# Performance work log

Measured on AMD Instinct MI355X. Metric: run time of the kernel, lower is better.

## Reference

```python
import jax, jax.numpy as jnp
import numpy as np
import math

B, H, L, DK = 4, 16, 4096, 64
LK0 = 4096
LOG_LK = int(math.log(LK0))  # 8
LOG_L = int(math.log(L))     # 8
NC = 3
D_MODEL = H * DK             # 1024


def setup_inputs() -> dict:
    key = jax.random.key(0)
    ks = jax.random.split(key, 20)
    s = 0.02  # small init scale for stability of softmax/clustering
    f = jnp.float32
    return dict(
        Q=jax.random.normal(ks[0], (B, H, L, DK), f),
        K=jax.random.normal(ks[1], (B, H, LK0, DK), f),
        V=jax.random.normal(ks[2], (B, H, LK0, DK), f),
        shrink_k_w=jax.random.normal(ks[3], (LOG_LK, LK0), f) * s,
        shrink_k_b=jax.random.normal(ks[4], (LOG_LK,), f) * s,
        shrink_v_w=jax.random.normal(ks[5], (LOG_LK, LK0), f) * s,
        shrink_v_b=jax.random.normal(ks[6], (LOG_LK,), f) * s,
        shrink_q_w=jax.random.normal(ks[7], (LOG_L, L), f) * s,
        shrink_q_b=jax.random.normal(ks[8], (LOG_L,), f) * s,
        pk_w=jax.random.normal(ks[9], (NC, LOG_LK * D_MODEL), f) * s,
        pk_b=jax.random.normal(ks[10], (NC,), f) * s,
        pq_w=jax.random.normal(ks[11], (NC, LOG_L * D_MODEL), f) * s,
        pq_b=jax.random.normal(ks[12], (NC,), f) * s,
        qp_w=jax.random.normal(ks[13], (NC, NC), f) * s,
        qp_b=jax.random.normal(ks[14], (NC,), f) * s,
        kp_w=jax.random.normal(ks[15], (NC, NC), f) * s,
        kp_b=jax.random.normal(ks[16], (NC,), f) * s,
    )


def reference(Q, K, V, shrink_k_w, shrink_k_b, shrink_v_w, shrink_v_b,
              shrink_q_w, shrink_q_b, pk_w, pk_b, pq_w, pq_b,
              qp_w, qp_b, kp_w, kp_b):
    b, h, l, d_k = Q.shape
    # shrink along sequence axis (Linear over seq after permute in torch)
    Ks = jnp.einsum('bhkd,mk->bhmd', K, shrink_k_w) + shrink_k_b[None, None, :, None]
    Vs = jnp.einsum('bhkd,mk->bhmd', V, shrink_v_w) + shrink_v_b[None, None, :, None]
    Qs = jnp.einsum('bhqd,mq->bhmd', Q, shrink_q_w) + shrink_q_b[None, None, :, None]
    lk = Ks.shape[2]  # = LOG_LK
    # cluster logits -> soft assignments
    ckp = jax.nn.relu(Ks.reshape(b, -1) @ pk_w.T + pk_b)
    cqp = jax.nn.relu(Qs.reshape(b, -1) @ pq_w.T + pq_b)
    cluster_q = jax.nn.softmax(cqp @ qp_w.T + qp_b, axis=-1)
    cluster_k = jax.nn.softmax(ckp @ kp_w.T + kp_b, axis=-1)
    mu = jnp.mean(cluster_q, axis=0)
    sigma = jax.nn.softplus(jnp.std(cluster_k, axis=0, ddof=1))  # torch.std is unbiased
    logp = -0.5 * jnp.square((cluster_k - mu) / sigma) - jnp.log(sigma) - 0.5 * jnp.log(2.0 * jnp.pi)
    # CrossEntropyLoss with soft targets: -mean_b sum_c target*log_softmax(input)
    ce = jnp.mean(-jnp.sum(cluster_q * jax.nn.log_softmax(cluster_q, axis=-1), axis=-1))
    loss = -jnp.mean(logp) + ce

    inds_q = jnp.argmax(cluster_q, axis=-1)  # [b]
    inds_k = jnp.argmax(cluster_k, axis=-1)  # [b]
    # get_group masks whole batches whose cluster == i+1 (per-batch constant mask;
    # the reshape round-trip in the original is an identity on [b,h,seq,d])
    mask_tril = jnp.tril(jnp.ones((l, lk), dtype=bool))  # True positions get -1e9
    nc = qp_b.shape[0]
    scores_center = jnp.zeros((nc, b, h, l, lk), Q.dtype)
    row_idx = jnp.broadcast_to(inds_q[:, None, None], (b, h, l))  # q_ind[:,:,:,0]
    bi = jnp.arange(b)[:, None, None]
    hi = jnp.arange(h)[None, :, None]
    scale = 1.0 / jnp.sqrt(jnp.asarray(d_k, Q.dtype))
    for i in range(nc):
        gQ = jnp.where((inds_q != i + 1)[:, None, None, None], Q, 0.0)
        gK = jnp.where((inds_k != i + 1)[:, None, None, None], Ks, 0.0)
        s = jnp.einsum('bhqd,bhkd->bhqk', gQ, gK) * scale  # [b,h,l,lk]
        s = jnp.where(mask_tril, -1e9, s)
        # original repeats gK lk times along a c-axis, softmaxes, then means over c:
        # all c-copies are identical, so mean over c == the per-copy value; then [0]
        sm0 = jax.nn.softmax(s, axis=-1)[0]  # [h,l,lk] (batch 0, as in original)
        scores_center = scores_center.at[i, bi, hi, row_idx, :].set(
            jnp.broadcast_to(sm0, (b, h, l, lk)))
    final_score = jnp.max(scores_center, axis=0)  # [b,h,l,lk]
    attn = jax.nn.softmax(final_score, axis=-1)
    context = jnp.einsum('bhqk,bhkd->bhqd', attn, Vs)
    return context, loss
```

## Files before the change

### kernel.cpp

```cpp
#include <hip/hip_runtime.h>
#include <hip/hip_bf16.h>
#include <math.h>

#define BB   4
#define HH   16
#define LL   4096
#define DKK  64
#define MM   8
#define NCC  3
#define BH   (BB*HH)
#define NCHUNK 8
#define ROWS_PER_CHUNK (LL/NCHUNK)
#define NSLOT 4
#define CTX_ELEMS (BB*HH*LL*DKK)

#define DOTS_OFF (3*BH*NSLOT*512)

__global__ __launch_bounds__(256, 6) void shrink_kernel(
    const float* __restrict__ Q, const float* __restrict__ K,
    const float* __restrict__ V,
    const float* __restrict__ skw, const float* __restrict__ svw,
    const float* __restrict__ sqw,
    float* __restrict__ ws)
{
    __shared__ float wlds[MM * ROWS_PER_CHUNK];
    float* red = wlds;

    int bx    = blockIdx.x;
    int input = bx >> 9;
    int rem   = bx & 511;
    int bh    = rem >> 3;
    int chunk = rem & 7;

    const float* X; const float* W;
    if (input == 0)      { X = K; W = skw; }
    else if (input == 1) { X = V; W = svw; }
    else                 { X = Q; W = sqw; }

    int t  = threadIdx.x;
    int k0 = chunk * ROWS_PER_CHUNK;

    {
        int mhalf = t >> 7;
        int idx   = (t & 127) * 4;
        #pragma unroll
        for (int mm = 0; mm < 4; ++mm) {
            int m = mm*2 + mhalf;
            *reinterpret_cast<float4*>(&wlds[m*ROWS_PER_CHUNK + idx]) =
                *reinterpret_cast<const float4*>(&W[m*LL + k0 + idx]);
        }
    }
    __syncthreads();

    int dg     = t & 15;
    int d4     = dg * 4;
    int stripe = t >> 4;

    const float* base = X + (size_t)bh * LL * DKK + (size_t)k0 * DKK;

    float4 acc[MM];
    #pragma unroll
    for (int m = 0; m < MM; ++m) acc[m] = make_float4(0.f, 0.f, 0.f, 0.f);

    for (int j = 0; j < ROWS_PER_CHUNK/128; ++j) {
        float4 v[8];
        #pragma unroll
        for (int u = 0; u < 8; ++u) {
            int row = j*128 + u*16 + stripe;
            v[u] = *reinterpret_cast<const float4*>(base + (size_t)row * DKK + d4);
        }
        #pragma unroll
        for (int u = 0; u < 8; ++u) {
            int row = j*128 + u*16 + stripe;
            #pragma unroll
            for (int m = 0; m < MM; ++m) {
                float w = wlds[m*ROWS_PER_CHUNK + row];
                acc[m].x = fmaf(v[u].x, w, acc[m].x);
                acc[m].y = fmaf(v[u].y, w, acc[m].y);
                acc[m].z = fmaf(v[u].z, w, acc[m].z);
                acc[m].w = fmaf(v[u].w, w, acc[m].w);
            }
        }
    }

    #pragma unroll
    for (int m = 0; m < MM; ++m) {
        acc[m].x += __shfl_xor(acc[m].x, 16);
        acc[m].y += __shfl_xor(acc[m].y, 16);
        acc[m].z += __shfl_xor(acc[m].z, 16);
        acc[m].w += __shfl_xor(acc[m].w, 16);
        acc[m].x += __shfl_xor(acc[m].x, 32);
        acc[m].y += __shfl_xor(acc[m].y, 32);
        acc[m].z += __shfl_xor(acc[m].z, 32);
        acc[m].w += __shfl_xor(acc[m].w, 32);
    }

    __syncthreads();

    int wave = t >> 6, lane = t & 63;
    if (lane < 16) {
        float* r = &red[(wave*16 + lane) * 33];
        #pragma unroll
        for (int m = 0; m < MM; ++m) {
            r[m*4 + 0] = acc[m].x;
            r[m*4 + 1] = acc[m].y;
            r[m*4 + 2] = acc[m].z;
            r[m*4 + 3] = acc[m].w;
        }
    }
    __syncthreads();

    float* wsb = ws + (size_t)(((input*BH + bh)*NSLOT + (chunk & 3))) * 512;
    for (int o = t; o < 512; o += 256) {
        int m = o >> 6, d = o & 63;
        int dgg = d >> 2, dc = d & 3;
        float s = 0.f;
        #pragma unroll
        for (int w = 0; w < 4; ++w)
            s += red[(w*16 + dgg)*33 + m*4 + dc];
        atomicAdd(wsb + o, s);
    }
}

__global__ __launch_bounds__(256) void dot_kernel(
    const float* __restrict__ ws,
    const float* __restrict__ skb, const float* __restrict__ sqb,
    const float* __restrict__ pk_w, const float* __restrict__ pk_b,
    const float* __restrict__ pq_w, const float* __restrict__ pq_b,
    float* __restrict__ dots)
{
    __shared__ float red[4];
    int idx = blockIdx.x;
    int isQ = idx >= 12;
    int g   = idx - (isQ ? 12 : 0);
    int b   = g / NCC;
    int c   = g % NCC;

    int input = isQ ? 2 : 0;
    const float* pw   = (isQ ? pq_w : pk_w) + (size_t)c * 8192;
    const float* bias = isQ ? sqb : skb;

    float bl[MM];
    #pragma unroll
    for (int m = 0; m < MM; ++m) bl[m] = bias[m];

    int t = threadIdx.x;
    float acc = 0.f;
    #pragma unroll
    for (int i = 0; i < 8; ++i) {
        int e = i*256 + t;
        int h = e >> 7;
        int m = (e >> 4) & 7;
        const float* xb = ws + (size_t)(((input*BH + b*HH + h)*NSLOT)) * 512
                             + (size_t)(e & 127) * 4;
        float4 x = make_float4(0.f, 0.f, 0.f, 0.f);
        #pragma unroll
        for (int ch = 0; ch < NSLOT; ++ch) {
            float4 p = *reinterpret_cast<const float4*>(xb + ch*512);
            x.x += p.x; x.y += p.y; x.z += p.z; x.w += p.w;
        }
        float4 w = *reinterpret_cast<const float4*>(pw + (size_t)e * 4);
        float bm = bl[m];
        acc = fmaf(x.x + bm, w.x, acc);
        acc = fmaf(x.y + bm, w.y, acc);
        acc = fmaf(x.z + bm, w.z, acc);
        acc = fmaf(x.w + bm, w.w, acc);
    }
    #pragma unroll
    for (int off = 1; off < 64; off <<= 1) acc += __shfl_xor(acc, off);
    int wave = t >> 6, lane = t & 63;
    if (lane == 0) red[wave] = acc;
    __syncthreads();
    if (t == 0) {
        float total = red[0] + red[1] + red[2] + red[3];
        float pb = (isQ ? pq_b : pk_b)[c];
        float r  = total + pb;
        dots[idx] = r > 0.f ? r : 0.f;
    }
}

__global__ __launch_bounds__(64) void final_kernel(
    const float* __restrict__ dots,
    const float* __restrict__ qp_w, const float* __restrict__ qp_b,
    const float* __restrict__ kp_w, const float* __restrict__ kp_b,
    float* __restrict__ out_loss)
{
    __shared__ float s_dots[24];
    __shared__ float s_qpw[9], s_qpb[3], s_kpw[9], s_kpb[3];
    int t = threadIdx.x;
    if (t < 24) s_dots[t] = dots[t];
    if (t < 9)  { s_qpw[t] = qp_w[t]; s_kpw[t] = kp_w[t]; }
    if (t < 3)  { s_qpb[t] = qp_b[t]; s_kpb[t] = kp_b[t]; }
    __syncthreads();

    if (t == 0) {
        float cq[BB][NCC], ck[BB][NCC];
        for (int b = 0; b < BB; ++b) {
            float lq[NCC], lk[NCC];
            for (int c = 0; c < NCC; ++c) {
                float sq = s_qpb[c], sk = s_kpb[c];
                for (int c2 = 0; c2 < NCC; ++c2) {
                    sq = fmaf(s_dots[12 + b*NCC + c2], s_qpw[c*NCC + c2], sq);
                    sk = fmaf(s_dots[b*NCC + c2],      s_kpw[c*NCC + c2], sk);
                }
                lq[c] = sq; lk[c] = sk;
            }
            float mq = fmaxf(fmaxf(lq[0], lq[1]), lq[2]);
            float mk = fmaxf(fmaxf(lk[0], lk[1]), lk[2]);
            float zq = 0.f, zk = 0.f;
            for (int c = 0; c < NCC; ++c) {
                cq[b][c] = expf(lq[c] - mq); zq += cq[b][c];
                ck[b][c] = expf(lk[c] - mk); zk += ck[b][c];
            }
            for (int c = 0; c < NCC; ++c) { cq[b][c] /= zq; ck[b][c] /= zk; }
        }
        float mu[NCC], mk_[NCC], sigma[NCC];
        for (int c = 0; c < NCC; ++c) {
            float s1 = 0.f, s2 = 0.f;
            for (int b = 0; b < BB; ++b) { s1 += cq[b][c]; s2 += ck[b][c]; }
            mu[c]  = s1 * 0.25f;
            mk_[c] = s2 * 0.25f;
        }
        for (int c = 0; c < NCC; ++c) {
            float v = 0.f;
            for (int b = 0; b < BB; ++b) {
                float d = ck[b][c] - mk_[c];
                v = fmaf(d, d, v);
            }
            float stdv = sqrtf(v / (BB - 1));
            sigma[c] = log1pf(expf(stdv));
        }
        const float HALF_LOG_2PI = 0.9189385332046727f;
        float sum_logp = 0.f;
        for (int b = 0; b < BB; ++b)
            for (int c = 0; c < NCC; ++c) {
                float z = (ck[b][c] - mu[c]) / sigma[c];
                sum_logp += -0.5f*z*z - logf(sigma[c]) - HALF_LOG_2PI;
            }
        float ce = 0.f;
        for (int b = 0; b < BB; ++b) {
            float mx = fmaxf(fmaxf(cq[b][0], cq[b][1]), cq[b][2]);
            float z = 0.f;
            for (int c = 0; c < NCC; ++c) z += expf(cq[b][c] - mx);
            float lse = mx + logf(z);
            float s = 0.f;
            for (int c = 0; c < NCC; ++c) s += cq[b][c] * (cq[b][c] - lse);
            ce += -s;
        }
        ce *= 0.25f;
        float loss = -(sum_logp / (BB * NCC)) + ce;
        out_loss[0] = loss;
    }
}

__global__ __launch_bounds__(256) void broadcast_kernel(
    const float* __restrict__ ws, const float* __restrict__ svb,
    float* __restrict__ out)
{
    int bx = blockIdx.x;
    int bh = bx >> 4;
    int lc = bx & 15;
    int t  = threadIdx.x;
    int d4     = (t & 15) * 4;
    int stripe = t >> 4;

    const float* vsb = ws + (size_t)((1*BH + bh)*NSLOT) * 512;
    float bias = 0.f;
    #pragma unroll
    for (int m = 0; m < MM; ++m) bias += svb[m];
    bias *= 0.125f;

    float4 c = make_float4(bias, bias, bias, bias);
    #pragma unroll
    for (int m = 0; m < MM; ++m) {
        #pragma unroll
        for (int ch = 0; ch < NSLOT; ++ch) {
            const float* p = vsb + ch*512 + m*64 + d4;
            c.x += 0.125f * p[0];
            c.y += 0.125f * p[1];
            c.z += 0.125f * p[2];
            c.w += 0.125f * p[3];
        }
    }

    float* obase = out + (size_t)bh * LL * DKK + (size_t)lc * 256 * DKK;
    #pragma unroll
    for (int i = 0; i < 16; ++i) {
        int l = i*16 + stripe;
        *reinterpret_cast<float4*>(obase + (size_t)l * DKK + d4) = c;
    }
}

extern "C" void kernel_launch(void* const* d_in, const int* in_sizes, int n_in,
                              void* d_out, int out_size, void* d_ws, size_t ws_size,
                              hipStream_t stream) {
    const float* Q    = (const float*)d_in[0];
    const float* K    = (const float*)d_in[1];
    const float* V    = (const float*)d_in[2];
    const float* skw  = (const float*)d_in[3];
    const float* skb  = (const float*)d_in[4];
    const float* svw  = (const float*)d_in[5];
    const float* svb  = (const float*)d_in[6];
    const float* sqw  = (const float*)d_in[7];
    const float* sqb  = (const float*)d_in[8];
    const float* pk_w = (const float*)d_in[9];
    const float* pk_b = (const float*)d_in[10];
    const float* pq_w = (const float*)d_in[11];
    const float* pq_b = (const float*)d_in[12];
    const float* qp_w = (const float*)d_in[13];
    const float* qp_b = (const float*)d_in[14];
    const float* kp_w = (const float*)d_in[15];
    const float* kp_b = (const float*)d_in[16];

    float* out = (float*)d_out;
    float* ws  = (float*)d_ws;

    hipMemsetAsync(ws, 0, (size_t)DOTS_OFF * sizeof(float), stream);

    shrink_kernel<<<dim3(3 * BH * NCHUNK), dim3(256), 0, stream>>>(
        Q, K, V, skw, svw, sqw, ws);

    dot_kernel<<<dim3(24), dim3(256), 0, stream>>>(
        ws, skb, sqb, pk_w, pk_b, pq_w, pq_b, ws + DOTS_OFF);

    final_kernel<<<dim3(1), dim3(64), 0, stream>>>(
        ws + DOTS_OFF, qp_w, qp_b, kp_w, kp_b, out + (size_t)CTX_ELEMS);

    broadcast_kernel<<<dim3(BH * 16), dim3(256), 0, stream>>>(ws, svb, out);
}
```

Before: 272.7 us.

## Drop memset and atomics in shrink, fuse final loss into broadcast kernel

Each shrink block now processes two 512-row chunks (c and c+4) and writes its own workspace slot directly, so the workspace memset and the atomicAdds go away. The final loss computation becomes an extra block in the broadcast kernel, removing one launch. Halving the shrink grid to 768 blocks gives fewer blocks and a longer serial loop per block, which could reduce latency hiding on the memory-bound reduction.

```diff
diff --git a/kernel.cpp b/kernel.cpp
--- a/kernel.cpp
+++ b/kernel.cpp
@@ -9,14 +9,13 @@
 #define MM   8
 #define NCC  3
 #define BH   (BB*HH)
-#define NCHUNK 8
-#define ROWS_PER_CHUNK (LL/NCHUNK)
 #define NSLOT 4
+#define ROWS_PER_CHUNK 512
 #define CTX_ELEMS (BB*HH*LL*DKK)
 
 #define DOTS_OFF (3*BH*NSLOT*512)
 
-__global__ __launch_bounds__(256, 6) void shrink_kernel(
+__global__ __launch_bounds__(256) void shrink_kernel(
     const float* __restrict__ Q, const float* __restrict__ K,
     const float* __restrict__ V,
     const float* __restrict__ skw, const float* __restrict__ svw,
@@ -27,60 +26,64 @@
     float* red = wlds;
 
     int bx    = blockIdx.x;
-    int input = bx >> 9;
-    int rem   = bx & 511;
-    int bh    = rem >> 3;
-    int chunk = rem & 7;
+    int input = bx >> 8;
+    int rem   = bx & 255;
+    int bh    = rem >> 2;
+    int c     = rem & 3;
 
     const float* X; const float* W;
     if (input == 0)      { X = K; W = skw; }
     else if (input == 1) { X = V; W = svw; }
     else                 { X = Q; W = sqw; }
 
-    int t  = threadIdx.x;
-    int k0 = chunk * ROWS_PER_CHUNK;
-
-    {
-        int mhalf = t >> 7;
-        int idx   = (t & 127) * 4;
-        #pragma unroll
-        for (int mm = 0; mm < 4; ++mm) {
-            int m = mm*2 + mhalf;
-            *reinterpret_cast<float4*>(&wlds[m*ROWS_PER_CHUNK + idx]) =
-                *reinterpret_cast<const float4*>(&W[m*LL + k0 + idx]);
-        }
-    }
-    __syncthreads();
-
+    int t      = threadIdx.x;
     int dg     = t & 15;
     int d4     = dg * 4;
     int stripe = t >> 4;
 
-    const float* base = X + (size_t)bh * LL * DKK + (size_t)k0 * DKK;
-
     float4 acc[MM];
     #pragma unroll
     for (int m = 0; m < MM; ++m) acc[m] = make_float4(0.f, 0.f, 0.f, 0.f);
 
-    for (int j = 0; j < ROWS_PER_CHUNK/128; ++j) {
-        float4 v[8];
-        #pragma unroll
-        for (int u = 0; u < 8; ++u) {
-            int row = j*128 + u*16 + stripe;
-            v[u] = *reinterpret_cast<const float4*>(base + (size_t)row * DKK + d4);
-        }
-        #pragma unroll
-        for (int u = 0; u < 8; ++u) {
-            int row = j*128 + u*16 + stripe;
+    #pragma unroll
+    for (int half = 0; half < 2; ++half) {
+        int k0 = (c + half*4) * ROWS_PER_CHUNK;
+
+        {
+            int mhalf = t >> 7;
+            int idx   = (t & 127) * 4;
             #pragma unroll
-            for (int m = 0; m < MM; ++m) {
-                float w = wlds[m*ROWS_PER_CHUNK + row];
-                acc[m].x = fmaf(v[u].x, w, acc[m].x);
-                acc[m].y = fmaf(v[u].y, w, acc[m].y);
-                acc[m].z = fmaf(v[u].z, w, acc[m].z);
-                acc[m].w = fmaf(v[u].w, w, acc[m].w);
-            }
-        }
+            for (int mm = 0; mm < 4; ++mm) {
+                int m = mm*2 + mhalf;
+                *reinterpret_cast<float4*>(&wlds[m*ROWS_PER_CHUNK + idx]) =
+                    *reinterpret_cast<const float4*>(&W[m*LL + k0 + idx]);
+            }
+        }
+        __syncthreads();
+
+        const float* base = X + (size_t)bh * LL * DKK + (size_t)k0 * DKK;
+
+        for (int j = 0; j < ROWS_PER_CHUNK/128; ++j) {
+            float4 v[8];
+            #pragma unroll
+            for (int u = 0; u < 8; ++u) {
+                int row = j*128 + u*16 + stripe;
+                v[u] = *reinterpret_cast<const float4*>(base + (size_t)row * DKK + d4);
+            }
+            #pragma unroll
+            for (int u = 0; u < 8; ++u) {
+                int row = j*128 + u*16 + stripe;
+                #pragma unroll
+                for (int m = 0; m < MM; ++m) {
+                    float w = wlds[m*ROWS_PER_CHUNK + row];
+                    acc[m].x = fmaf(v[u].x, w, acc[m].x);
+                    acc[m].y = fmaf(v[u].y, w, acc[m].y);
+                    acc[m].z = fmaf(v[u].z, w, acc[m].z);
+                    acc[m].w = fmaf(v[u].w, w, acc[m].w);
+                }
+            }
+        }
+        __syncthreads();
     }
 
     #pragma unroll
@@ -95,8 +98,6 @@
         acc[m].w += __shfl_xor(acc[m].w, 32);
     }
 
-    __syncthreads();
-
     int wave = t >> 6, lane = t & 63;
     if (lane < 16) {
         float* r = &red[(wave*16 + lane) * 33];
@@ -110,7 +111,7 @@
     }
     __syncthreads();
 
-    float* wsb = ws + (size_t)(((input*BH + bh)*NSLOT + (chunk & 3))) * 512;
+    float* wsb = ws + (size_t)(((input*BH + bh)*NSLOT + c)) * 512;
     for (int o = t; o < 512; o += 256) {
         int m = o >> 6, d = o & 63;
         int dgg = d >> 2, dc = d & 3;
@@ -118,7 +119,7 @@
         #pragma unroll
         for (int w = 0; w < 4; ++w)
             s += red[(w*16 + dgg)*33 + m*4 + dc];
-        atomicAdd(wsb + o, s);
+        wsb[o] = s;
     }
 }
 
@@ -179,88 +180,85 @@
     }
 }
 
-__global__ __launch_bounds__(64) void final_kernel(
+__global__ __launch_bounds__(256) void broadcast_final_kernel(
+    const float* __restrict__ ws, const float* __restrict__ svb,
     const float* __restrict__ dots,
     const float* __restrict__ qp_w, const float* __restrict__ qp_b,
     const float* __restrict__ kp_w, const float* __restrict__ kp_b,
-    float* __restrict__ out_loss)
-{
-    __shared__ float s_dots[24];
-    __shared__ float s_qpw[9], s_qpb[3], s_kpw[9], s_kpb[3];
-    int t = threadIdx.x;
-    if (t < 24) s_dots[t] = dots[t];
-    if (t < 9)  { s_qpw[t] = qp_w[t]; s_kpw[t] = kp_w[t]; }
-    if (t < 3)  { s_qpb[t] = qp_b[t]; s_kpb[t] = kp_b[t]; }
-    __syncthreads();
-
-    if (t == 0) {
-        float cq[BB][NCC], ck[BB][NCC];
-        for (int b = 0; b < BB; ++b) {
-            float lq[NCC], lk[NCC];
-            for (int c = 0; c < NCC; ++c) {
-                float sq = s_qpb[c], sk = s_kpb[c];
-                for (int c2 = 0; c2 < NCC; ++c2) {
-                    sq = fmaf(s_dots[12 + b*NCC + c2], s_qpw[c*NCC + c2], sq);
-                    sk = fmaf(s_dots[b*NCC + c2],      s_kpw[c*NCC + c2], sk);
-                }
-                lq[c] = sq; lk[c] = sk;
-            }
-            float mq = fmaxf(fmaxf(lq[0], lq[1]), lq[2]);
-            float mk = fmaxf(fmaxf(lk[0], lk[1]), lk[2]);
-            float zq = 0.f, zk = 0.f;
-            for (int c = 0; c < NCC; ++c) {
-                cq[b][c] = expf(lq[c] - mq); zq += cq[b][c];
-                ck[b][c] = expf(lk[c] - mk); zk += ck[b][c];
-            }
-            for (int c = 0; c < NCC; ++c) { cq[b][c] /= zq; ck[b][c] /= zk; }
-        }
-        float mu[NCC], mk_[NCC], sigma[NCC];
-        for (int c = 0; c < NCC; ++c) {
-            float s1 = 0.f, s2 = 0.f;
-            for (int b = 0; b < BB; ++b) { s1 += cq[b][c]; s2 += ck[b][c]; }
-            mu[c]  = s1 * 0.25f;
-            mk_[c] = s2 * 0.25f;
-        }
-        for (int c = 0; c < NCC; ++c) {
-            float v = 0.f;
-            for (int b = 0; b < BB; ++b) {
-                float d = ck[b][c] - mk_[c];
-                v = fmaf(d, d, v);
-            }
-            float stdv = sqrtf(v / (BB - 1));
-            sigma[c] = log1pf(expf(stdv));
-        }
-        const float HALF_LOG_2PI = 0.9189385332046727f;
-        float sum_logp = 0.f;
-        for (int b = 0; b < BB; ++b)
-            for (int c = 0; c < NCC; ++c) {
-                float z = (ck[b][c] - mu[c]) / sigma[c];
-                sum_logp += -0.5f*z*z - logf(sigma[c]) - HALF_LOG_2PI;
-            }
-        float ce = 0.f;
-        for (int b = 0; b < BB; ++b) {
-            float mx = fmaxf(fmaxf(cq[b][0], cq[b][1]), cq[b][2]);
-            float z = 0.f;
-            for (int c = 0; c < NCC; ++c) z += expf(cq[b][c] - mx);
-            float lse = mx + logf(z);
-            float s = 0.f;
-            for (int c = 0; c < NCC; ++c) s += cq[b][c] * (cq[b][c] - lse);
-            ce += -s;
-        }
-        ce *= 0.25f;
-        float loss = -(sum_logp / (BB * NCC)) + ce;
-        out_loss[0] = loss;
-    }
-}
-
-__global__ __launch_bounds__(256) void broadcast_kernel(
-    const float* __restrict__ ws, const float* __restrict__ svb,
     float* __restrict__ out)
 {
     int bx = blockIdx.x;
+    int t  = threadIdx.x;
+
+    if (bx == BH * 16) {
+        __shared__ float s_dots[24];
+        __shared__ float s_qpw[9], s_qpb[3], s_kpw[9], s_kpb[3];
+        if (t < 24) s_dots[t] = dots[t];
+        if (t < 9)  { s_qpw[t] = qp_w[t]; s_kpw[t] = kp_w[t]; }
+        if (t < 3)  { s_qpb[t] = qp_b[t]; s_kpb[t] = kp_b[t]; }
+        __syncthreads();
+        if (t == 0) {
+            float cq[BB][NCC], ck[BB][NCC];
+            for (int b = 0; b < BB; ++b) {
+                float lq[NCC], lk[NCC];
+                for (int c = 0; c < NCC; ++c) {
+                    float sq = s_qpb[c], sk = s_kpb[c];
+                    for (int c2 = 0; c2 < NCC; ++c2) {
+                        sq = fmaf(s_dots[12 + b*NCC + c2], s_qpw[c*NCC + c2], sq);
+                        sk = fmaf(s_dots[b*NCC + c2],      s_kpw[c*NCC + c2], sk);
+                    }
+                    lq[c] = sq; lk[c] = sk;
+                }
+                float mq = fmaxf(fmaxf(lq[0], lq[1]), lq[2]);
+                float mk = fmaxf(fmaxf(lk[0], lk[1]), lk[2]);
+                float zq = 0.f, zk = 0.f;
+                for (int cc = 0; cc < NCC; ++cc) {
+                    cq[b][cc] = expf(lq[cc] - mq); zq += cq[b][cc];
+                    ck[b][cc] = expf(lk[cc] - mk); zk += ck[b][cc];
+                }
+                for (int cc = 0; cc < NCC; ++cc) { cq[b][cc] /= zq; ck[b][cc] /= zk; }
+            }
+            float mu[NCC], mk_[NCC], sigma[NCC];
+            for (int cc = 0; cc < NCC; ++cc) {
+                float s1 = 0.f, s2 = 0.f;
+                for (int b = 0; b < BB; ++b) { s1 += cq[b][cc]; s2 += ck[b][cc]; }
+                mu[cc]  = s1 * 0.25f;
+                mk_[cc] = s2 * 0.25f;
+            }
+            for (int cc = 0; cc < NCC; ++cc) {
+                float v = 0.f;
+                for (int b = 0; b < BB; ++b) {
+                    float d = ck[b][cc] - mk_[cc];
+                    v = fmaf(d, d, v);
+                }
+                float stdv = sqrtf(v / (BB - 1));
+                sigma[cc] = log1pf(expf(stdv));
+            }
+            const float HALF_LOG_2PI = 0.9189385332046727f;
+            float sum_logp = 0.f;
+            for (int b = 0; b < BB; ++b)
+                for (int cc = 0; cc < NCC; ++cc) {
+                    float z = (ck[b][cc] - mu[cc]) / sigma[cc];
+                    sum_logp += -0.5f*z*z - logf(sigma[cc]) - HALF_LOG_2PI;
+                }
+            float ce = 0.f;
+            for (int b = 0; b < BB; ++b) {
+                float mx = fmaxf(fmaxf(cq[b][0], cq[b][1]), cq[b][2]);
+                float z = 0.f;
+                for (int cc = 0; cc < NCC; ++cc) z += expf(cq[b][cc] - mx);
+                float lse = mx + logf(z);
+                float s = 0.f;
+                for (int cc = 0; cc < NCC; ++cc) s += cq[b][cc] * (cq[b][cc] - lse);
+                ce += -s;
+            }
+            ce *= 0.25f;
+            out[(size_t)CTX_ELEMS] = -(sum_logp / (BB * NCC)) + ce;
+        }
+        return;
+    }
+
     int bh = bx >> 4;
     int lc = bx & 15;
-    int t  = threadIdx.x;
     int d4     = (t & 15) * 4;
     int stripe = t >> 4;
 
@@ -270,16 +268,16 @@
     for (int m = 0; m < MM; ++m) bias += svb[m];
     bias *= 0.125f;
 
-    float4 c = make_float4(bias, bias, bias, bias);
+    float4 cc4 = make_float4(bias, bias, bias, bias);
     #pragma unroll
     for (int m = 0; m < MM; ++m) {
         #pragma unroll
         for (int ch = 0; ch < NSLOT; ++ch) {
             const float* p = vsb + ch*512 + m*64 + d4;
-            c.x += 0.125f * p[0];
-            c.y += 0.125f * p[1];
-            c.z += 0.125f * p[2];
-            c.w += 0.125f * p[3];
+            cc4.x += 0.125f * p[0];
+            cc4.y += 0.125f * p[1];
+            cc4.z += 0.125f * p[2];
+            cc4.w += 0.125f * p[3];
         }
     }
 
@@ -287,7 +285,7 @@
     #pragma unroll
     for (int i = 0; i < 16; ++i) {
         int l = i*16 + stripe;
-        *reinterpret_cast<float4*>(obase + (size_t)l * DKK + d4) = c;
+        *reinterpret_cast<float4*>(obase + (size_t)l * DKK + d4) = cc4;
     }
 }
 
@@ -315,16 +313,12 @@
     float* out = (float*)d_out;
     float* ws  = (float*)d_ws;
 
-    hipMemsetAsync(ws, 0, (size_t)DOTS_OFF * sizeof(float), stream);
-
-    shrink_kernel<<<dim3(3 * BH * NCHUNK), dim3(256), 0, stream>>>(
+    shrink_kernel<<<dim3(3 * BH * NSLOT), dim3(256), 0, stream>>>(
         Q, K, V, skw, svw, sqw, ws);
 
     dot_kernel<<<dim3(24), dim3(256), 0, stream>>>(
         ws, skb, sqb, pk_w, pk_b, pq_w, pq_b, ws + DOTS_OFF);
 
-    final_kernel<<<dim3(1), dim3(64), 0, stream>>>(
-        ws + DOTS_OFF, qp_w, qp_b, kp_w, kp_b, out + (size_t)CTX_ELEMS);
-
-    broadcast_kernel<<<dim3(BH * 16), dim3(256), 0, stream>>>(ws, svb, out);
+    broadcast_final_kernel<<<dim3(BH * 16 + 1), dim3(256), 0, stream>>>(
+        ws, svb, ws + DOTS_OFF, qp_w, qp_b, kp_w, kp_b, out);
 }
```

After: 263.6 us. -3.3%, faster.
